# Kernel optimization log

Hardware: AMD Instinct MI355X
Metric: run time of the kernel (lower is better)

## Reference

```python
import jax, jax.numpy as jnp
import numpy as np

N_HEADS = 16
HEAD_SIZE = 64

def setup_inputs() -> dict:
    key = jax.random.key(0)
    k1, k2 = jax.random.split(key)
    B, N, D = 2, 2048, N_HEADS * HEAD_SIZE
    x = jax.random.normal(k1, (B, N, D), dtype=jnp.float32)
    # lecun_normal-ish scale for the QKV kernel
    W_qkv = jax.random.normal(k2, (D, 3 * D), dtype=jnp.float32) * (1.0 / np.sqrt(D))
    return {"x": x, "W_qkv": W_qkv}

def reference(x, W_qkv):
    B, N, D = x.shape
    H, Dh = N_HEADS, HEAD_SIZE
    qkv = x @ W_qkv                                  # [B,N,3D]
    q, k, v = jnp.split(qkv, 3, axis=-1)
    q = q.reshape(B, N, H, Dh)
    k = k.reshape(B, N, H, Dh)
    v = v.reshape(B, N, H, Dh)
    dist = jnp.einsum('bihd,bjhd->bhij', q, k) / jnp.sqrt(jnp.asarray(Dh, dtype=x.dtype))
    mask = jnp.tril(jnp.ones((N, N), dtype=bool))[None, None, :, :]
    dist = jnp.where(mask, dist, -jnp.inf)
    attn = jax.nn.softmax(dist, axis=-1)             # [B,H,N,N]
    out_heads = jnp.einsum('bhij,bjhd->bihd', attn, v)
    return out_heads.reshape(B, N, H * Dh)
```

## Files before the change

### kernel.cpp

```cpp
#include <hip/hip_runtime.h>

typedef __attribute__((ext_vector_type(8))) short bf16x8;
typedef __attribute__((ext_vector_type(4))) float f32x4;
typedef __attribute__((ext_vector_type(16))) float f32x16;
typedef __attribute__((ext_vector_type(2))) unsigned int u32x2;

#define DEVI static __device__ __forceinline__

namespace {
constexpr int NSEQ = 2048, NH = 16;
constexpr int D = 1024, D3 = 3072;
}

DEVI unsigned short f2bf(float f) {
  union { float f; unsigned int u; } v; v.f = f;
  unsigned int r = v.u + 0x7FFFu + ((v.u >> 16) & 1u);
  return (unsigned short)(r >> 16);
}

DEVI void gload16(const unsigned short* g, unsigned short* lds_) {
  __builtin_amdgcn_global_load_lds(
      (const __attribute__((address_space(1))) unsigned int*)g,
      (__attribute__((address_space(3))) unsigned int*)lds_, 16, 0, 0);
}

DEVI f32x4 mfma16(bf16x8 a, bf16x8 b, f32x4 c) {
  return __builtin_amdgcn_mfma_f32_16x16x32_bf16(a, b, c, 0, 0, 0);
}

DEVI f32x16 mfma32(bf16x8 a, bf16x8 b, f32x16 c) {
  return __builtin_amdgcn_mfma_f32_32x32x16_bf16(a, b, c, 0, 0, 0);
}

DEVI float exp2g(float x) {
#if __has_builtin(__builtin_amdgcn_exp2f)
  return __builtin_amdgcn_exp2f(x);
#else
  return exp2f(x);
#endif
}

DEVI unsigned int cvtpk(float a, float b) {
  unsigned int r;
  asm("v_cvt_pk_bf16_f32 %0, %1, %2" : "=v"(r) : "v"(a), "v"(b));
  return r;
}

DEVI u32x2 pswap2(unsigned int a, unsigned int b) {
  return __builtin_amdgcn_permlane32_swap(a, b, false, false);
}
DEVI float xmax_halves(float v) {
  union { float f; unsigned int u; } c; c.f = v;
  u32x2 r = pswap2(c.u, c.u);
  union { unsigned int u; float f; } x, y; x.u = r.x; y.u = r.y;
  return fmaxf(x.f, y.f);
}
DEVI float xsum_halves(float v) {
  union { float f; unsigned int u; } c; c.f = v;
  u32x2 r = pswap2(c.u, c.u);
  union { unsigned int u; float f; } x, y; x.u = r.x; y.u = r.y;
  return x.f + y.f;
}

union U4 { unsigned int u[4]; bf16x8 v; };

__global__ __launch_bounds__(256) void prep_k(const float* __restrict__ x,
                                              const float* __restrict__ W,
                                              unsigned short* __restrict__ xb,
                                              unsigned short* __restrict__ Wt) {
  __shared__ float t[32][33];
  const int bid = blockIdx.x;
  if (bid < 4096) {
    int i = (bid * 256 + threadIdx.x) * 4;
    float4 v = *reinterpret_cast<const float4*>(x + i);
    ushort4 o;
    o.x = f2bf(v.x); o.y = f2bf(v.y); o.z = f2bf(v.z); o.w = f2bf(v.w);
    *reinterpret_cast<ushort4*>(xb + i) = o;
  } else {
    const int b2 = bid - 4096;
    const int c0 = (b2 % 96) * 32, k0 = (b2 / 96) * 32;
    const int tx = threadIdx.x & 31, ty = threadIdx.x >> 5;
#pragma unroll
    for (int r = 0; r < 32; r += 8)
      t[ty + r][tx] = W[(size_t)(k0 + ty + r) * D3 + c0 + tx];
    __syncthreads();
#pragma unroll
    for (int r = 0; r < 32; r += 8)
      Wt[(size_t)(c0 + ty + r) * D + k0 + tx] = f2bf(t[tx][ty + r]);
  }
}

__global__ __launch_bounds__(256) void qkv_gemm_k(const unsigned short* __restrict__ xb,
                                                  const unsigned short* __restrict__ Wt,
                                                  unsigned short* __restrict__ qw,
                                                  unsigned short* __restrict__ kw,
                                                  unsigned short* __restrict__ vtw) {
  __shared__ unsigned short smA[128 * 32];
  __shared__ unsigned short smB[128 * 32];
  const int tid = threadIdx.x, w = tid >> 6, l = tid & 63;
  const int m0 = blockIdx.x * 128, n0 = blockIdx.y * 128;
  const int wm = w >> 1, wn = w & 1;

  const unsigned short* ga[2]; const unsigned short* gb[2];
  unsigned short* la[2]; unsigned short* lb[2];
#pragma unroll
  for (int i = 0; i < 2; ++i) {
    int idx = tid + i * 256;
    int row = idx >> 2;
    int blk = (idx & 3) ^ ((row >> 1) & 3);
    ga[i] = xb + (size_t)(m0 + row) * D + blk * 8;
    gb[i] = Wt + (size_t)(n0 + row) * D + blk * 8;
    la[i] = smA + (w * 64 + i * 256) * 8;
    lb[i] = smB + (w * 64 + i * 256) * 8;
  }

  f32x4 acc[4][4];
#pragma unroll
  for (int a = 0; a < 4; ++a)
#pragma unroll
    for (int b = 0; b < 4; ++b) acc[a][b] = (f32x4){0.f, 0.f, 0.f, 0.f};

  for (int kt = 0; kt < D / 32; ++kt) {
    __syncthreads();
#pragma unroll
    for (int i = 0; i < 2; ++i) {
      gload16(ga[i] + kt * 32, la[i]);
      gload16(gb[i] + kt * 32, lb[i]);
    }
    asm volatile("s_waitcnt vmcnt(0)" ::: "memory");
    __syncthreads();

    bf16x8 af[4], bfr[4];
#pragma unroll
    for (int a = 0; a < 4; ++a) {
      int arow = wm * 64 + a * 16 + (l & 15);
      int blk = (l >> 4) ^ ((arow >> 1) & 3);
      af[a] = *reinterpret_cast<const bf16x8*>(smA + arow * 32 + blk * 8);
    }
#pragma unroll
    for (int b = 0; b < 4; ++b) {
      int brow = wn * 64 + b * 16 + (l & 15);
      int blk = (l >> 4) ^ ((brow >> 1) & 3);
      bfr[b] = *reinterpret_cast<const bf16x8*>(smB + brow * 32 + blk * 8);
    }
#pragma unroll
    for (int a = 0; a < 4; ++a)
#pragma unroll
      for (int b = 0; b < 4; ++b)
        acc[a][b] = mfma16(af[a], bfr[b], acc[a][b]);
  }

  const int which = n0 >> 10;
#pragma unroll
  for (int a = 0; a < 4; ++a) {
#pragma unroll
    for (int b = 0; b < 4; ++b) {
#pragma unroll
      for (int r = 0; r < 4; ++r) {
        int grow = m0 + wm * 64 + a * 16 + (l >> 4) * 4 + r;
        int gcol = n0 + wn * 64 + b * 16 + (l & 15);
        float v = acc[a][b][r];
        int bb = grow >> 11, n = grow & 2047;
        int cc = gcol & 1023, h = cc >> 6, dh = cc & 63;
        size_t bh = (size_t)bb * NH + h;
        if (which == 0)
          qw[(bh * NSEQ + n) * 64 + dh] = f2bf(v * 0.18033688011112042f);
        else if (which == 1)
          kw[(bh * NSEQ + n) * 64 + dh] = f2bf(v);
        else
          vtw[(bh * 64 + dh) * NSEQ + n] = f2bf(v);
      }
    }
  }
}

__global__ __launch_bounds__(256, 2) void attn_k(const unsigned short* __restrict__ qw,
                                                 const unsigned short* __restrict__ kw,
                                                 const unsigned short* __restrict__ vtw,
                                                 float* __restrict__ out) {
  __shared__ __align__(16) char lds[66560];
  const int tid = threadIdx.x, w = tid >> 6, l = tid & 63;
  const int hi = l >> 5, ql = l & 31;
  const int qsub = w >> 1, par = w & 1;

  const int wg = blockIdx.x;
  const int xcd = wg & 7, rest = wg >> 3;
  const int bhl = rest >> 4;
  const int j = rest & 15;
  const int bh = xcd * 4 + bhl;
  const int bb = bh >> 4, h = bh & 15;

  const unsigned short* qb = qw + (size_t)bh * NSEQ * 64;
  const unsigned short* kb = kw + (size_t)bh * NSEQ * 64;
  const unsigned short* vb = vtw + (size_t)bh * 64 * NSEQ;

  const int r0 = tid >> 3, c0 = (tid & 7) ^ (r0 & 7);
  const int r1 = (tid + 256) >> 3, c1 = ((tid + 256) & 7) ^ (r1 & 7);
  const int wbase = w * 512;

#define STAGE(SL, PR)                                                            \
  do {                                                                           \
    const int t0_ = 2 * (PR), t1_ = 2 * (PR) + 1;                                \
    unsigned short* k0d = (unsigned short*)(lds + (SL) * 32768) + wbase;         \
    unsigned short* v0d = (unsigned short*)(lds + (SL) * 32768 + 8192) + wbase;  \
    unsigned short* k1d = (unsigned short*)(lds + (SL) * 32768 + 16384) + wbase; \
    unsigned short* v1d = (unsigned short*)(lds + (SL) * 32768 + 24576) + wbase; \
    gload16(kb + (((size_t)t0_ * 64 + r0) * 64 + c0 * 8), k0d);                  \
    gload16(kb + (((size_t)t0_ * 64 + r1) * 64 + c1 * 8), k0d + 2048);           \
    gload16(vb + ((size_t)r0 * NSEQ + t0_ * 64 + c0 * 8), v0d);                  \
    gload16(vb + ((size_t)r1 * NSEQ + t0_ * 64 + c1 * 8), v0d + 2048);           \
    gload16(kb + (((size_t)t1_ * 64 + r0) * 64 + c0 * 8), k1d);                  \
    gload16(kb + (((size_t)t1_ * 64 + r1) * 64 + c1 * 8), k1d + 2048);           \
    gload16(vb + ((size_t)r0 * NSEQ + t1_ * 64 + c0 * 8), v1d);                  \
    gload16(vb + ((size_t)r1 * NSEQ + t1_ * 64 + c1 * 8), v1d + 2048);           \
  } while (0)

  for (int seg = 0; seg < 2; ++seg) {
    const int qt = seg ? j : (31 - j);
    const int qbase = qt * 64;
    const int qg = qbase + qsub * 32 + ql;

    bf16x8 qf[4];
#pragma unroll
    for (int ds = 0; ds < 4; ++ds)
      qf[ds] = *reinterpret_cast<const bf16x8*>(qb + (size_t)qg * 64 + ds * 16 + hi * 8);

    float m = -1e30f, lsum = 0.f;
    f32x16 O0, O1;
#pragma unroll
    for (int r2 = 0; r2 < 16; ++r2) { O0[r2] = 0.f; O1[r2] = 0.f; }

    const int nsup = (qt >> 1) + 1;
    STAGE(0, 0);
    for (int s = 0; s < nsup; ++s) {
      __syncthreads();
      if (s + 1 < nsup) STAGE((s + 1) & 1, s + 1);
      const int t = 2 * s + par;
      if (t <= qt) {
        const char* Kb = lds + (s & 1) * 32768 + par * 16384;
        const char* Vb = Kb + 8192;

        f32x16 S0, S1;
#pragma unroll
        for (int r2 = 0; r2 < 16; ++r2) { S0[r2] = 0.f; S1[r2] = 0.f; }
        __builtin_amdgcn_s_setprio(1);
#pragma unroll
        for (int ds = 0; ds < 4; ++ds) {
          bf16x8 k0 = *reinterpret_cast<const bf16x8*>(
              Kb + ql * 128 + (((2 * ds + hi) ^ (ql & 7)) << 4));
          bf16x8 k1 = *reinterpret_cast<const bf16x8*>(
              Kb + (32 + ql) * 128 + (((2 * ds + hi) ^ (ql & 7)) << 4));
          S0 = mfma32(k0, qf[ds], S0);
          S1 = mfma32(k1, qf[ds], S1);
        }
        __builtin_amdgcn_s_setprio(0);

        if (t == qt) {
#pragma unroll
          for (int reg = 0; reg < 16; ++reg) {
            const int krow = (reg & 3) + 8 * (reg >> 2) + 4 * hi;
            if (64 * t + krow > qg) S0[reg] = -1e30f;
            if (64 * t + 32 + krow > qg) S1[reg] = -1e30f;
          }
        }

        float t0 = fmaxf(S0[0], S1[0]), t1 = fmaxf(S0[1], S1[1]);
        float t2 = fmaxf(S0[2], S1[2]), t3 = fmaxf(S0[3], S1[3]);
#pragma unroll
        for (int r2 = 4; r2 < 16; r2 += 4) {
          t0 = fmaxf(t0, fmaxf(S0[r2], S1[r2]));
          t1 = fmaxf(t1, fmaxf(S0[r2 + 1], S1[r2 + 1]));
          t2 = fmaxf(t2, fmaxf(S0[r2 + 2], S1[r2 + 2]));
          t3 = fmaxf(t3, fmaxf(S0[r2 + 3], S1[r2 + 3]));
        }
        float tmax = xmax_halves(fmaxf(fmaxf(t0, t1), fmaxf(t2, t3)));

        if (!__all(tmax <= m + 8.0f)) {
          const float mn = fmaxf(m, tmax);
          const float g = exp2g(m - mn);
          m = mn;
          lsum *= g;
#pragma unroll
          for (int r2 = 0; r2 < 16; ++r2) { O0[r2] *= g; O1[r2] *= g; }
        }

        float pr0[16], pr1[16];
        float rA = 0.f, rB = 0.f, rC = 0.f, rD = 0.f;
#pragma unroll
        for (int r2 = 0; r2 < 16; r2 += 4) {
          pr0[r2] = exp2g(S0[r2] - m);     pr1[r2] = exp2g(S1[r2] - m);
          pr0[r2 + 1] = exp2g(S0[r2 + 1] - m); pr1[r2 + 1] = exp2g(S1[r2 + 1] - m);
          pr0[r2 + 2] = exp2g(S0[r2 + 2] - m); pr1[r2 + 2] = exp2g(S1[r2 + 2] - m);
          pr0[r2 + 3] = exp2g(S0[r2 + 3] - m); pr1[r2 + 3] = exp2g(S1[r2 + 3] - m);
          rA += pr0[r2] + pr1[r2];
          rB += pr0[r2 + 1] + pr1[r2 + 1];
          rC += pr0[r2 + 2] + pr1[r2 + 2];
          rD += pr0[r2 + 3] + pr1[r2 + 3];
        }
        lsum += xsum_halves((rA + rB) + (rC + rD));

        bf16x8 pf[4];
#pragma unroll
        for (int ct = 0; ct < 2; ++ct) {
          const float* pp = ct ? pr1 : pr0;
          unsigned int u[4][2];
#pragma unroll
          for (int c = 0; c < 4; ++c) {
            u[c][0] = cvtpk(pp[4 * c], pp[4 * c + 1]);
            u[c][1] = cvtpk(pp[4 * c + 2], pp[4 * c + 3]);
          }
#pragma unroll
          for (int kk = 0; kk < 2; ++kk) {
            u32x2 rw0 = pswap2(u[2 * kk][0], u[2 * kk + 1][0]);
            u32x2 rw1 = pswap2(u[2 * kk][1], u[2 * kk + 1][1]);
            U4 f;
            f.u[0] = rw0.x; f.u[1] = rw1.x;
            f.u[2] = rw0.y; f.u[3] = rw1.y;
            pf[2 * ct + kk] = f.v;
          }
        }

        __builtin_amdgcn_s_setprio(1);
#pragma unroll
        for (int ks = 0; ks < 4; ++ks) {
          bf16x8 v0 = *reinterpret_cast<const bf16x8*>(
              Vb + ql * 128 + (((2 * ks + hi) ^ (ql & 7)) << 4));
          bf16x8 v1 = *reinterpret_cast<const bf16x8*>(
              Vb + (32 + ql) * 128 + (((2 * ks + hi) ^ (ql & 7)) << 4));
          O0 = mfma32(v0, pf[ks], O0);
          O1 = mfma32(v1, pf[ks], O1);
        }
        __builtin_amdgcn_s_setprio(0);
      }
    }

    __syncthreads();
    float* mlp = (float*)(lds + 65536);
    if (l < 32) { mlp[w * 64 + l] = m; mlp[w * 64 + 32 + l] = lsum; }
    __syncthreads();
    {
      const int pw = w ^ 1;
      const float m1 = mlp[pw * 64 + ql];
      const float l1 = mlp[pw * 64 + 32 + ql];
      const float M = fmaxf(m, m1);
      const float g0 = exp2g(m - M);
      const float g1 = exp2g(m1 - M);
      const float L = lsum * g0 + l1 * g1;
      const float phi = g0 / L;
      float* mo = (float*)lds + (qsub * 2 + par) * 2048;
#pragma unroll
      for (int reg = 0; reg < 16; ++reg) {
        const int dr = (reg & 3) + 8 * (reg >> 2) + 4 * hi;
        const int d1 = 32 + dr;
        mo[ql * 64 + (((dr >> 2) ^ (ql & 7)) << 2) + (dr & 3)] = O0[reg] * phi;
        mo[ql * 64 + (((d1 >> 2) ^ (ql & 7)) << 2) + (d1 & 3)] = O1[reg] * phi;
      }
    }
    __syncthreads();
    {
      const int qq = tid >> 2, dq = (tid & 3) << 4;
      const float* pa = (float*)lds + ((qq >> 5) * 2 + 0) * 2048 + (qq & 31) * 64;
      const float* pb = (float*)lds + ((qq >> 5) * 2 + 1) * 2048 + (qq & 31) * 64;
      float* op = out + ((size_t)bb * NSEQ + qbase + qq) * D + h * 64 + dq;
#pragma unroll
      for (int c = 0; c < 4; ++c) {
        const int ch = ((dq >> 2) + c) ^ (qq & 7);
        float4 va = *reinterpret_cast<const float4*>(pa + ch * 4);
        float4 vb4 = *reinterpret_cast<const float4*>(pb + ch * 4);
        float4 s4 = make_float4(va.x + vb4.x, va.y + vb4.y, va.z + vb4.z, va.w + vb4.w);
        *reinterpret_cast<float4*>(op + c * 4) = s4;
      }
    }
    __syncthreads();
  }
#undef STAGE
}

extern "C" void kernel_launch(void* const* d_in, const int* in_sizes, int n_in,
                              void* d_out, int out_size, void* d_ws, size_t ws_size,
                              hipStream_t stream) {
  const float* x = (const float*)d_in[0];
  const float* W = (const float*)d_in[1];
  float* out = (float*)d_out;
  char* ws = (char*)d_ws;
  unsigned short* xb  = (unsigned short*)(ws);
  unsigned short* Wt  = (unsigned short*)(ws + 8388608);
  unsigned short* qw  = (unsigned short*)(ws + 14680064);
  unsigned short* kw  = (unsigned short*)(ws + 23068672);
  unsigned short* vtw = (unsigned short*)(ws + 31457280);

  prep_k<<<7168, 256, 0, stream>>>(x, W, xb, Wt);
  qkv_gemm_k<<<dim3(32, 24), 256, 0, stream>>>(xb, Wt, qw, kw, vtw);
  attn_k<<<512, 256, 0, stream>>>(qw, kw, vtw, out);
}
```

Measured before the change: 85.09 us.

## Split each query tile's KV range across four waves per group with 512-thread blocks

```diff
diff --git a/kernel.cpp b/kernel.cpp
--- a/kernel.cpp
+++ b/kernel.cpp
@@ -54,12 +54,6 @@
   u32x2 r = pswap2(c.u, c.u);
   union { unsigned int u; float f; } x, y; x.u = r.x; y.u = r.y;
   return fmaxf(x.f, y.f);
-}
-DEVI float xsum_halves(float v) {
-  union { float f; unsigned int u; } c; c.f = v;
-  u32x2 r = pswap2(c.u, c.u);
-  union { unsigned int u; float f; } x, y; x.u = r.x; y.u = r.y;
-  return x.f + y.f;
 }
 
 union U4 { unsigned int u[4]; bf16x8 v; };
@@ -174,14 +168,14 @@
   }
 }
 
-__global__ __launch_bounds__(256, 2) void attn_k(const unsigned short* __restrict__ qw,
+__global__ __launch_bounds__(512, 4) void attn_k(const unsigned short* __restrict__ qw,
                                                  const unsigned short* __restrict__ kw,
                                                  const unsigned short* __restrict__ vtw,
                                                  float* __restrict__ out) {
-  __shared__ __align__(16) char lds[66560];
+  __shared__ __align__(16) char lds[67584];
   const int tid = threadIdx.x, w = tid >> 6, l = tid & 63;
   const int hi = l >> 5, ql = l & 31;
-  const int qsub = w >> 1, par = w & 1;
+  const int qsub = w >> 2, par = w & 3;
 
   const int wg = blockIdx.x;
   const int xcd = wg & 7, rest = wg >> 3;
@@ -194,25 +188,23 @@
   const unsigned short* kb = kw + (size_t)bh * NSEQ * 64;
   const unsigned short* vb = vtw + (size_t)bh * 64 * NSEQ;
 
-  const int r0 = tid >> 3, c0 = (tid & 7) ^ (r0 & 7);
-  const int r1 = (tid + 256) >> 3, c1 = ((tid + 256) & 7) ^ (r1 & 7);
-  const int wbase = w * 512;
-
-#define STAGE(SL, PR)                                                            \
-  do {                                                                           \
-    const int t0_ = 2 * (PR), t1_ = 2 * (PR) + 1;                                \
-    unsigned short* k0d = (unsigned short*)(lds + (SL) * 32768) + wbase;         \
-    unsigned short* v0d = (unsigned short*)(lds + (SL) * 32768 + 8192) + wbase;  \
-    unsigned short* k1d = (unsigned short*)(lds + (SL) * 32768 + 16384) + wbase; \
-    unsigned short* v1d = (unsigned short*)(lds + (SL) * 32768 + 24576) + wbase; \
-    gload16(kb + (((size_t)t0_ * 64 + r0) * 64 + c0 * 8), k0d);                  \
-    gload16(kb + (((size_t)t0_ * 64 + r1) * 64 + c1 * 8), k0d + 2048);           \
-    gload16(vb + ((size_t)r0 * NSEQ + t0_ * 64 + c0 * 8), v0d);                  \
-    gload16(vb + ((size_t)r1 * NSEQ + t0_ * 64 + c1 * 8), v0d + 2048);           \
-    gload16(kb + (((size_t)t1_ * 64 + r0) * 64 + c0 * 8), k1d);                  \
-    gload16(kb + (((size_t)t1_ * 64 + r1) * 64 + c1 * 8), k1d + 2048);           \
-    gload16(vb + ((size_t)r0 * NSEQ + t1_ * 64 + c0 * 8), v1d);                  \
-    gload16(vb + ((size_t)r1 * NSEQ + t1_ * 64 + c1 * 8), v1d + 2048);           \
+  const int sr = tid >> 3, sc = (tid & 7) ^ (sr & 7);
+
+#define STAGE4(TB)                                                              \
+  do {                                                                          \
+    _Pragma("unroll")                                                           \
+    for (int i_ = 0; i_ < 8; ++i_) {                                            \
+      const int T_ = i_ >> 1, kv_ = i_ & 1;                                     \
+      const int gt_ = (TB) + T_;                                                \
+      if (gt_ <= qt) {                                                          \
+        unsigned short* d_ =                                                    \
+            (unsigned short*)(lds + T_ * 16384 + kv_ * 8192) + w * 512;         \
+        if (kv_ == 0)                                                           \
+          gload16(kb + ((size_t)(gt_ * 64 + sr) * 64 + sc * 8), d_);            \
+        else                                                                    \
+          gload16(vb + ((size_t)sr * NSEQ + gt_ * 64 + sc * 8), d_);            \
+      }                                                                         \
+    }                                                                           \
   } while (0)
 
   for (int seg = 0; seg < 2; ++seg) {
@@ -230,14 +222,17 @@
 #pragma unroll
     for (int r2 = 0; r2 < 16; ++r2) { O0[r2] = 0.f; O1[r2] = 0.f; }
 
-    const int nsup = (qt >> 1) + 1;
-    STAGE(0, 0);
+    const int nsup = (qt >> 2) + 1;
     for (int s = 0; s < nsup; ++s) {
+      const int tb = 4 * s;
       __syncthreads();
-      if (s + 1 < nsup) STAGE((s + 1) & 1, s + 1);
-      const int t = 2 * s + par;
+      STAGE4(tb);
+      asm volatile("s_waitcnt vmcnt(0)" ::: "memory");
+      __syncthreads();
+
+      const int t = tb + par;
       if (t <= qt) {
-        const char* Kb = lds + (s & 1) * 32768 + par * 16384;
+        const char* Kb = lds + par * 16384;
         const char* Vb = Kb + 8192;
 
         f32x16 S0, S1;
@@ -284,30 +279,39 @@
           for (int r2 = 0; r2 < 16; ++r2) { O0[r2] *= g; O1[r2] *= g; }
         }
 
-        float pr0[16], pr1[16];
         float rA = 0.f, rB = 0.f, rC = 0.f, rD = 0.f;
 #pragma unroll
         for (int r2 = 0; r2 < 16; r2 += 4) {
-          pr0[r2] = exp2g(S0[r2] - m);     pr1[r2] = exp2g(S1[r2] - m);
-          pr0[r2 + 1] = exp2g(S0[r2 + 1] - m); pr1[r2 + 1] = exp2g(S1[r2 + 1] - m);
-          pr0[r2 + 2] = exp2g(S0[r2 + 2] - m); pr1[r2 + 2] = exp2g(S1[r2 + 2] - m);
-          pr0[r2 + 3] = exp2g(S0[r2 + 3] - m); pr1[r2 + 3] = exp2g(S1[r2 + 3] - m);
-          rA += pr0[r2] + pr1[r2];
-          rB += pr0[r2 + 1] + pr1[r2 + 1];
-          rC += pr0[r2 + 2] + pr1[r2 + 2];
-          rD += pr0[r2 + 3] + pr1[r2 + 3];
-        }
-        lsum += xsum_halves((rA + rB) + (rC + rD));
+          S0[r2] = exp2g(S0[r2] - m);         S1[r2] = exp2g(S1[r2] - m);
+          S0[r2 + 1] = exp2g(S0[r2 + 1] - m); S1[r2 + 1] = exp2g(S1[r2 + 1] - m);
+          S0[r2 + 2] = exp2g(S0[r2 + 2] - m); S1[r2 + 2] = exp2g(S1[r2 + 2] - m);
+          S0[r2 + 3] = exp2g(S0[r2 + 3] - m); S1[r2 + 3] = exp2g(S1[r2 + 3] - m);
+          rA += S0[r2] + S1[r2];
+          rB += S0[r2 + 1] + S1[r2 + 1];
+          rC += S0[r2 + 2] + S1[r2 + 2];
+          rD += S0[r2 + 3] + S1[r2 + 3];
+        }
+        {
+          float rsum = (rA + rB) + (rC + rD);
+          union { float f; unsigned int u; } c; c.f = rsum;
+          u32x2 r = pswap2(c.u, c.u);
+          union { unsigned int u; float f; } x, y; x.u = r.x; y.u = r.y;
+          lsum += x.f + y.f;
+        }
 
         bf16x8 pf[4];
 #pragma unroll
         for (int ct = 0; ct < 2; ++ct) {
-          const float* pp = ct ? pr1 : pr0;
           unsigned int u[4][2];
 #pragma unroll
           for (int c = 0; c < 4; ++c) {
-            u[c][0] = cvtpk(pp[4 * c], pp[4 * c + 1]);
-            u[c][1] = cvtpk(pp[4 * c + 2], pp[4 * c + 3]);
+            if (ct == 0) {
+              u[c][0] = cvtpk(S0[4 * c], S0[4 * c + 1]);
+              u[c][1] = cvtpk(S0[4 * c + 2], S0[4 * c + 3]);
+            } else {
+              u[c][0] = cvtpk(S1[4 * c], S1[4 * c + 1]);
+              u[c][1] = cvtpk(S1[4 * c + 2], S1[4 * c + 3]);
+            }
           }
 #pragma unroll
           for (int kk = 0; kk < 2; ++kk) {
@@ -339,15 +343,16 @@
     if (l < 32) { mlp[w * 64 + l] = m; mlp[w * 64 + 32 + l] = lsum; }
     __syncthreads();
     {
-      const int pw = w ^ 1;
-      const float m1 = mlp[pw * 64 + ql];
-      const float l1 = mlp[pw * 64 + 32 + ql];
-      const float M = fmaxf(m, m1);
-      const float g0 = exp2g(m - M);
-      const float g1 = exp2g(m1 - M);
-      const float L = lsum * g0 + l1 * g1;
-      const float phi = g0 / L;
-      float* mo = (float*)lds + (qsub * 2 + par) * 2048;
+      float M = m, L = 0.f;
+#pragma unroll
+      for (int q = 0; q < 4; ++q)
+        M = fmaxf(M, mlp[(qsub * 4 + q) * 64 + ql]);
+#pragma unroll
+      for (int q = 0; q < 4; ++q)
+        L += mlp[(qsub * 4 + q) * 64 + 32 + ql] *
+             exp2g(mlp[(qsub * 4 + q) * 64 + ql] - M);
+      const float phi = exp2g(m - M) / L;
+      float* mo = (float*)(lds + w * 8192);
 #pragma unroll
       for (int reg = 0; reg < 16; ++reg) {
         const int dr = (reg & 3) + 8 * (reg >> 2) + 4 * hi;
@@ -358,22 +363,26 @@
     }
     __syncthreads();
     {
-      const int qq = tid >> 2, dq = (tid & 3) << 4;
-      const float* pa = (float*)lds + ((qq >> 5) * 2 + 0) * 2048 + (qq & 31) * 64;
-      const float* pb = (float*)lds + ((qq >> 5) * 2 + 1) * 2048 + (qq & 31) * 64;
+      const int qq = tid >> 3;
+      const int dq = (tid & 7) * 8;
+      const int qsr = qq >> 5, qrow = qq & 31;
       float* op = out + ((size_t)bb * NSEQ + qbase + qq) * D + h * 64 + dq;
 #pragma unroll
-      for (int c = 0; c < 4; ++c) {
-        const int ch = ((dq >> 2) + c) ^ (qq & 7);
-        float4 va = *reinterpret_cast<const float4*>(pa + ch * 4);
-        float4 vb4 = *reinterpret_cast<const float4*>(pb + ch * 4);
-        float4 s4 = make_float4(va.x + vb4.x, va.y + vb4.y, va.z + vb4.z, va.w + vb4.w);
-        *reinterpret_cast<float4*>(op + c * 4) = s4;
+      for (int c2 = 0; c2 < 2; ++c2) {
+        const int ch = ((dq >> 2) + c2) ^ (qrow & 7);
+        float4 s4 = make_float4(0.f, 0.f, 0.f, 0.f);
+#pragma unroll
+        for (int p = 0; p < 4; ++p) {
+          const float* bufp = (const float*)(lds + (qsr * 4 + p) * 8192);
+          float4 v = *reinterpret_cast<const float4*>(bufp + qrow * 64 + ch * 4);
+          s4.x += v.x; s4.y += v.y; s4.z += v.z; s4.w += v.w;
+        }
+        *reinterpret_cast<float4*>(op + c2 * 4) = s4;
       }
     }
     __syncthreads();
   }
-#undef STAGE
+#undef STAGE4
 }
 
 extern "C" void kernel_launch(void* const* d_in, const int* in_sizes, int n_in,
@@ -391,5 +400,5 @@
 
   prep_k<<<7168, 256, 0, stream>>>(x, W, xb, Wt);
   qkv_gemm_k<<<dim3(32, 24), 256, 0, stream>>>(xb, Wt, qw, kw, vtw);
-  attn_k<<<512, 256, 0, stream>>>(qw, kw, vtw, out);
-}
+  attn_k<<<512, 512, 0, stream>>>(qw, kw, vtw, out);
+}
```

Result: slower. 90.40 us (+6.2%).
